# Kernel tuning notes

Hardware: AMD Instinct MI355X
Metric: run time of the kernel (lower is better)

Reference implementation:

```python
import jax, jax.numpy as jnp
import numpy as np
import math

H, N2, RANK, CH, LMAX = 256, 64, 1, 1, 2048
DT_MIN, DT_MAX = 1e-3, 1e-1


def setup_inputs() -> dict:
    key = jax.random.key(0)
    kP, kPi, kC, kCi, kdt = jax.random.split(key, 5)
    # DPLR 'lin' init: A = -1/2 - i*pi*n  (real_part=0.5, imag_part=pi*arange(N//2))
    A_real = 0.5 * jnp.ones((H, N2), jnp.float32)
    A_imag = math.pi * jnp.broadcast_to(jnp.arange(N2, dtype=jnp.float32), (H, N2))
    # B_init='constant': B = ones (complex)
    B_real = jnp.ones((H, N2), jnp.float32)
    B_imag = jnp.zeros((H, N2), jnp.float32)
    # P = randn complex (rank, H, N//2); torch complex randn has per-component std 1/sqrt(2)
    s = 1.0 / math.sqrt(2.0)
    P_real = s * jax.random.normal(kP, (RANK, H, N2), jnp.float32)
    P_imag = s * jax.random.normal(kPi, (RANK, H, N2), jnp.float32)
    # C (output projection) randn complex (channels, H, N//2)
    C_real = s * jax.random.normal(kC, (CH, H, N2), jnp.float32)
    C_imag = s * jax.random.normal(kCi, (CH, H, N2), jnp.float32)
    # dt log-uniform in [dt_min, dt_max]
    log_dt = math.log(DT_MIN) + jax.random.uniform(kdt, (H,), jnp.float32) * (
        math.log(DT_MAX) - math.log(DT_MIN))
    return {
        "A_real": A_real, "A_imag": A_imag,
        "B_real": B_real, "B_imag": B_imag,
        "P_real": P_real, "P_imag": P_imag,
        "C_real": C_real, "C_imag": C_imag,
        "log_dt": log_dt, "L": LMAX,
    }


def _krylov_doubling(dA, dB, L):
    """Matrix-power doubling scan (mirrors `power`): columns [dB, dA dB, ..., dA^{L-1} dB].

    dA: (H, N, N) complex, dB: (H, N) complex -> (H, N, L) complex.
    """
    x = dB[..., None]  # (H, N, 1)
    Ap = dA
    while x.shape[-1] < L:
        x = jnp.concatenate([x, Ap @ x], axis=-1)  # doubling step
        Ap = Ap @ Ap  # repeated squaring, as in power()
    return x[..., :L]


def reference(A_real, A_imag, B_real, B_imag, P_real, P_imag, C_real, C_imag, log_dt, L):
    # Build DPLR state matrix: A = diag(Lambda) - P P^*
    Lam = (-A_real - 1j * A_imag).astype(jnp.complex64)        # (H, N2)
    P = (P_real + 1j * P_imag).astype(jnp.complex64)           # (R, H, N2)
    B = (B_real + 1j * B_imag).astype(jnp.complex64)           # (H, N2)
    C = (C_real + 1j * C_imag).astype(jnp.complex64)           # (CH, H, N2)
    n2 = Lam.shape[-1]
    I = jnp.eye(n2, dtype=jnp.complex64)
    A_mat = Lam[:, :, None] * I - jnp.einsum('rhn,rhm->hnm', P, jnp.conj(P))  # (H,N2,N2)
    dt = jnp.exp(log_dt).astype(jnp.complex64)                 # (H,)
    # Bilinear (Tustin) discretization: dA = (I - dt/2 A)^{-1}(I + dt/2 A), dB = (I - dt/2 A)^{-1} dt B
    half = 0.5 * dt[:, None, None] * A_mat
    M_bwd = I - half
    dA = jnp.linalg.solve(M_bwd, I + half)                     # (H,N2,N2)
    dB = jnp.linalg.solve(M_bwd, (dt[:, None] * B)[..., None])[..., 0]  # (H,N2)
    # Kernel via power-doubling Krylov scan, then project: K[c,h,l] = 2 Re(C dA^l dB)
    x = _krylov_doubling(dA, dB, L)                            # (H,N2,L)
    K = 2.0 * jnp.real(jnp.einsum('chn,hnl->chl', C, x))       # (CH,H,L)
    return K
```

## Files before the change

kernel.cpp:

```cpp
#include <hip/hip_runtime.h>


#define LL 2048

struct C2 { float re, im; };

__device__ __forceinline__ C2 cmul(C2 a, C2 b){ return {a.re*b.re - a.im*b.im, a.re*b.im + a.im*b.re}; }
__device__ __forceinline__ C2 cadd(C2 a, C2 b){ return {a.re+b.re, a.im+b.im}; }
__device__ __forceinline__ C2 csub(C2 a, C2 b){ return {a.re-b.re, a.im-b.im}; }
__device__ __forceinline__ C2 cinv(C2 a){ float s=1.0f/(a.re*a.re+a.im*a.im); return {a.re*s, -a.im*s}; }
__device__ __forceinline__ C2 cscale(float s, C2 a){ return {s*a.re, s*a.im}; }
__device__ __forceinline__ C2 ld2(float2 v){ return {v.x, v.y}; }
__device__ __forceinline__ float2 st2(C2 v){ return make_float2(v.re, v.im); }

template<int CTRL>
__device__ __forceinline__ float dpp_add(float x){
  int t = __builtin_amdgcn_update_dpp(0, __float_as_int(x), CTRL, 0xF, 0xF, true);
  return x + __int_as_float(t);
}
__device__ __forceinline__ float wave_sum63(float x){
  x = dpp_add<0xB1>(x);
  x = dpp_add<0x4E>(x);
  x = dpp_add<0x124>(x);
  x = dpp_add<0x128>(x);
  x = dpp_add<0x142>(x);
  x = dpp_add<0x143>(x);
  return x;
}
__device__ __forceinline__ float bcast63(float x){
  return __int_as_float(__builtin_amdgcn_readlane(__float_as_int(x), 63));
}
__device__ __forceinline__ float rdlane(float v, int l){
  return __int_as_float(__builtin_amdgcn_readlane(__float_as_int(v), l));
}
__device__ __forceinline__ float shr1(float x){
  return __int_as_float(__builtin_amdgcn_update_dpp(0, __float_as_int(x), 0x138, 0xF, 0xF, true));
}
__device__ __forceinline__ float ins0(float v, float s, int lane){
  return (lane == 0) ? s : v;
}

__device__ __forceinline__ void tri_solve64(const C2 wl, C2 va, const int lane,
                                            float& so_re, float& so_im)
{
    C2 wsh = { shr1(wl.re), shr1(wl.im) };
    const float w0r = rdlane(wl.re, 0);
    const float w0i = rdlane(wl.im, 0);
    so_re = 0.0f; so_im = 0.0f;
    for (int j = 0; j < 64; j += 2) {
        const float s0r = rdlane(va.re, j);
        const float s0i = rdlane(va.im, j);
        const float v1r = rdlane(va.re, j + 1);
        const float v1i = rdlane(va.im, j + 1);
        const float s1r = v1r + (w0r*s0r - w0i*s0i);
        const float s1i = v1i + (w0r*s0i + w0i*s0r);
        if (lane == j)     { so_re = s0r; so_im = s0i; }
        if (lane == j + 1) { so_re = s1r; so_im = s1i; }
        const C2 wsh1 = { shr1(wsh.re), shr1(wsh.im) };
        va.re += wsh.re*s0r - wsh.im*s0i;
        va.im += wsh.re*s0i + wsh.im*s0r;
        va.re += wsh1.re*s1r - wsh1.im*s1i;
        va.im += wsh1.re*s1i + wsh1.im*s1r;
        wsh.re = shr1(wsh1.re);
        wsh.im = shr1(wsh1.im);
    }
}

__device__ __forceinline__ void tri_solve128(const C2 wlo, const C2 whi, const int lane,
                                             C2& tlo, C2& thi)
{
    C2 valo = wlo, vahi = whi;
    C2 wsl = { shr1(wlo.re), shr1(wlo.im) };
    C2 wsh;
    {
        const float br = rdlane(wlo.re, 63), bi = rdlane(wlo.im, 63);
        wsh.re = ins0(shr1(whi.re), br, lane);
        wsh.im = ins0(shr1(whi.im), bi, lane);
    }
    const float w0r = rdlane(wlo.re, 0);
    const float w0i = rdlane(wlo.im, 0);
    tlo = {0,0}; thi = {0,0};
    for (int j = 0; j < 64; j += 2) {
        const float s0r = rdlane(valo.re, j);
        const float s0i = rdlane(valo.im, j);
        const float v1r = rdlane(valo.re, j + 1);
        const float v1i = rdlane(valo.im, j + 1);
        const float s1r = v1r + (w0r*s0r - w0i*s0i);
        const float s1i = v1i + (w0r*s0i + w0i*s0r);
        if (lane == j)     { tlo.re = s0r; tlo.im = s0i; }
        if (lane == j + 1) { tlo.re = s1r; tlo.im = s1i; }
        const C2 wsl1 = { shr1(wsl.re), shr1(wsl.im) };
        C2 wsh1;
        {
            const float br = rdlane(wsl.re, 63), bi = rdlane(wsl.im, 63);
            wsh1.re = ins0(shr1(wsh.re), br, lane);
            wsh1.im = ins0(shr1(wsh.im), bi, lane);
        }
        valo.re += wsl.re*s0r - wsl.im*s0i + wsl1.re*s1r - wsl1.im*s1i;
        valo.im += wsl.re*s0i + wsl.im*s0r + wsl1.re*s1i + wsl1.im*s1r;
        vahi.re += wsh.re*s0r - wsh.im*s0i + wsh1.re*s1r - wsh1.im*s1i;
        vahi.im += wsh.re*s0i + wsh.im*s0r + wsh1.re*s1i + wsh1.im*s1r;
        wsl.re = shr1(wsl1.re); wsl.im = shr1(wsl1.im);
        {
            const float br = rdlane(wsl1.re, 63), bi = rdlane(wsl1.im, 63);
            wsh.re = ins0(shr1(wsh1.re), br, lane);
            wsh.im = ins0(shr1(wsh1.im), bi, lane);
        }
    }
    for (int j = 64; j < 128; j += 2) {
        const int jr = j - 64;
        const float s0r = rdlane(vahi.re, jr);
        const float s0i = rdlane(vahi.im, jr);
        const float v1r = rdlane(vahi.re, jr + 1);
        const float v1i = rdlane(vahi.im, jr + 1);
        const float s1r = v1r + (w0r*s0r - w0i*s0i);
        const float s1i = v1i + (w0r*s0i + w0i*s0r);
        if (lane == jr)     { thi.re = s0r; thi.im = s0i; }
        if (lane == jr + 1) { thi.re = s1r; thi.im = s1i; }
        const C2 wsh1 = { shr1(wsh.re), shr1(wsh.im) };
        vahi.re += wsh.re*s0r - wsh.im*s0i + wsh1.re*s1r - wsh1.im*s1i;
        vahi.im += wsh.re*s0i + wsh.im*s0r + wsh1.re*s1i + wsh1.im*s1r;
        wsh.re = shr1(wsh1.re);
        wsh.im = shr1(wsh1.im);
    }
}

__global__ __launch_bounds__(512)
__attribute__((amdgpu_waves_per_eu(2, 2)))
void ssm_dplr_kernel(
    const float* __restrict__ A_real, const float* __restrict__ A_imag,
    const float* __restrict__ B_real, const float* __restrict__ B_imag,
    const float* __restrict__ P_real, const float* __restrict__ P_imag,
    const float* __restrict__ C_real, const float* __restrict__ C_imag,
    const float* __restrict__ log_dt, float* __restrict__ out)
{
    const int h    = blockIdx.x;
    const int t    = threadIdx.x;
    const int lane = t & 63;
    const int wid  = t >> 6;

    extern __shared__ char sm[];
    float2* Abuf = (float2*)sm;
    float2* Cs   = (float2*)(sm + 32768);
    float2* tw   = Cs;
    float2* ta   = Cs + 512;
    float2* te   = Cs + 1024;
    float2* gA   = (float2*)(sm + 49152);
    float2* qA   = gA + 64;
    float2* g64A = gA + 128;
    float2* TgA  = gA + 192;
    float2* TpA  = gA + 256;
    float2* T1gA = gA + 320;
    float2* T1pA = gA + 384;
    char* ovl = sm + 52736;
    float2* rqA  = (float2*)ovl;
    float2* rxA  = rqA + 64;
    float2* reA  = rqA + 128;
    float2* wvA  = rqA + 192;
    float2* avA  = rqA + 256;
    float2* weA  = rqA + 320;
    float2* cbufAll = (float2*)ovl;
    float2* prtC    = (float2*)(sm + 56832);
    int*    cntA    = (int*)(sm + 65024);
    int*    cntB    = cntA + 32;

    const int idx = h * 64 + lane;
    const float dt = expf(log_dt[h]);
    const float c  = 0.5f * dt;

    const C2 lam = { -A_real[idx], -A_imag[idx] };
    const C2 p   = {  P_real[idx],  P_imag[idx] };
    const C2 Bv  = {  B_real[idx],  B_imag[idx] };
    const C2 Cv  = {  C_real[idx],  C_imag[idx] };
    const C2 pc  = { p.re, -p.im };

    const C2 d = cinv(C2{ 1.0f - c*lam.re, -c*lam.im });
    const C2 g = cmul(d, C2{ 1.0f + c*lam.re, c*lam.im });

    C2 sv = cscale(p.re*p.re + p.im*p.im, d);
    C2 uv = cmul(cmul(d, pc), Bv);
    sv.re = bcast63(wave_sum63(sv.re)); sv.im = bcast63(wave_sum63(sv.im));
    uv.re = bcast63(wave_sum63(uv.re)); uv.im = bcast63(wave_sum63(uv.im));

    const C2 beta  = cscale(c, cinv(C2{ 1.0f + c*sv.re, c*sv.im }));
    const C2 bs    = cmul(beta, sv);
    const C2 gamma = { -c*(1.0f - bs.re), c*bs.im };

    const C2 q  = cmul(d, p);
    const C2 r  = cmul(pc, csub(gamma, cmul(beta, g)));
    const C2 x0 = cscale(dt, csub(cmul(d, Bv), cmul(cmul(beta, uv), q)));

    const C2 g2  = cmul(g,  g);
    const C2 g4  = cmul(g2, g2);
    const C2 g8  = cmul(g4, g4);
    const C2 g16 = cmul(g8, g8);
    const C2 g32 = cmul(g16,g16);
    const C2 g64 = cmul(g32,g32);

    if (wid == 0) {
        const C2 rq = cmul(r, q);
        gA[lane]   = st2(g);
        qA[lane]   = st2(q);
        g64A[lane] = st2(g64);
        rqA[lane]  = st2(rq);
        rxA[lane]  = st2(cmul(r, x0));
        reA[lane]  = st2(cmul(rq, g64));
    }
    __syncthreads();

    {
        C2 cur = {1.0f, 0.0f};
        if (wid & 1) cur = g8;
        if (wid & 2) cur = cmul(cur, g16);
        if (wid & 4) cur = cmul(cur, g32);
        #pragma unroll
        for (int jj = 0; jj < 8; ++jj) {
            const int j = 8*wid + jj;
            Abuf[j*64 + ((lane + j) & 63)] = st2(cur);
            cur = cmul(cur, g);
        }
    }
    __syncthreads();

    {
        C2 accw = {0,0}, acca = {0,0}, acce = {0,0};
        #pragma unroll
        for (int kk = 0; kk < 8; ++kk) {
            const int n = 8*wid + kk;
            const C2 Gv = ld2(Abuf[lane*64 + ((n + lane) & 63)]);
            const C2 fq = ld2(rqA[n]);
            const C2 fx = ld2(rxA[n]);
            const C2 fe = ld2(reA[n]);
            accw = cadd(accw, cmul(Gv, fq));
            acca = cadd(acca, cmul(Gv, fx));
            acce = cadd(acce, cmul(Gv, fe));
        }
        tw[wid*64 + lane] = st2(accw);
        ta[wid*64 + lane] = st2(acca);
        te[wid*64 + lane] = st2(acce);
    }
    __syncthreads();
    if (t < 64) {
        C2 sw = {0,0}, sa = {0,0}, se = {0,0};
        #pragma unroll
        for (int w2 = 0; w2 < 8; ++w2) {
            sw = cadd(sw, ld2(tw[w2*64 + t]));
            sa = cadd(sa, ld2(ta[w2*64 + t]));
            se = cadd(se, ld2(te[w2*64 + t]));
        }
        wvA[t] = st2(sw);
        avA[t] = st2(sa);
        weA[t] = st2(se);
    }
    __syncthreads();

    const bool isB = (wid >= 4);
    const int  wg  = wid & 3;
    if (wid == 0) {
        C2 tlo, thi;
        tri_solve128(ld2(wvA[lane]), ld2(weA[lane]), lane, tlo, thi);
        C2 pp = { rdlane(tlo.re, 0),  rdlane(tlo.im, 0)  };
        C2 dd = {0,0};
        C2 qq = { rdlane(tlo.re, 63), rdlane(tlo.im, 63) };
        C2 qd = {0,0};
        for (int i = 1; i <= 63; ++i) {
            if (i <= 62) {
                const C2 ti = { rdlane(tlo.re, i), rdlane(tlo.im, i) };
                dd = cadd(cmul(dd, g), pp);
                pp = cadd(cmul(pp, g), ti);
            }
            const C2 tq = { rdlane(thi.re, i-1), rdlane(thi.im, i-1) };
            qd = cadd(cmul(qd, g), qq);
            qq = cadd(cmul(qq, g), tq);
        }
        const C2 T64v = cmul(g, pp);
        const C2 T64d = cadd(pp, cmul(g, dd));
        const C2 g63h  = cmul(g64, cinv(g));
        const C2 T128v = cadd(cmul(g64, T64v), cmul(g, qq));
        const C2 T128d = cadd(cadd(cscale(64.0f, cmul(g63h, T64v)), cmul(g64, T64d)),
                              cadd(qq, cmul(g, qd)));
        TgA[lane]  = st2(T64v);
        TpA[lane]  = st2(T64d);
        T1gA[lane] = st2(T128v);
        T1pA[lane] = st2(T128d);
    } else if (wid == 1) {
        float sg_re, sg_im;
        tri_solve64(ld2(wvA[lane]), ld2(avA[lane]), lane, sg_re, sg_im);
        C2 x = x0;
        for (int j = 0; j < 64; ++j) {
            Abuf[j*64 + ((lane + j) & 63)] = st2(x);
            const float sjr = rdlane(sg_re, j);
            const float sji = rdlane(sg_im, j);
            const float nr = g.re*x.re - g.im*x.im + sjr*q.re - sji*q.im;
            const float ni = g.re*x.im + g.im*x.re + sjr*q.im + sji*q.re;
            x.re = nr; x.im = ni;
        }
    }
    __syncthreads();

    C2 Mk[16];
    auto buildM = [&](bool p128){
        const C2 gt   = p128 ? cmul(g64, g64) : g64;
        const C2 Ttm  = p128 ? ld2(T1gA[lane]) : ld2(TgA[lane]);
        const C2 Tp   = p128 ? ld2(T1pA[lane]) : ld2(TpA[lane]);
        const C2 g63  = cmul(g64, cinv(g));
        const C2 gtm1 = p128 ? cmul(g64, g63) : g63;
        const C2 S    = cmul(r, cadd(cscale(p128 ? 128.0f : 64.0f, gtm1), Tp));
        const C2 diagv = cadd(gt, cmul(q, S));
        #pragma unroll
        for (int kk = 0; kk < 16; ++kk) {
            const int k = 16*wg + kk;
            const C2 qn   = ld2(qA[k]);
            const C2 g64n = ld2(g64A[k]);
            const C2 gtn  = p128 ? cmul(g64n, g64n) : g64n;
            const C2 Ttn  = p128 ? ld2(T1gA[k]) : ld2(TgA[k]);
            const C2 idm  = cinv(csub(ld2(gA[k]), g));
            const C2 num  = cmul(r, cadd(csub(gtn, gt), csub(Ttn, Ttm)));
            const C2 off  = cmul(cmul(qn, num), idm);
            const bool isd = (lane == k);
            Mk[kk].re = isd ? diagv.re : off.re;
            Mk[kk].im = isd ? diagv.im : off.im;
        }
    };
    if (!isB) buildM(true);
    else      buildM(false);
    if (wid == 0) Cs[lane] = st2(Cv);
    if (wid == 2) {
        if (lane < 32) cntA[lane] = 0;
        else           cntB[lane - 32] = 0;
    }
    __syncthreads();

    {
        float2* cb = cbufAll + wid*64;
        const float4* cb4 = (const float4*)cb;
        volatile int* vcnt = isB ? (volatile int*)cntB : (volatile int*)cntA;
        int* cnt = isB ? cntB : cntA;
        const int base = isB ? 4 : 0;
        cb[lane] = st2(Cv);

        const int s0 = isB ? 0 : 1;
        for (int s = s0; s <= 15; ++s) {
            const int buf = s & 1;
            float ar = 0.0f, ai = 0.0f;
            #pragma unroll
            for (int kp = 0; kp < 8; ++kp) {
                const float4 cc = cb4[8*wg + kp];
                ar += cc.x*Mk[2*kp].re   - cc.y*Mk[2*kp].im;
                ai += cc.x*Mk[2*kp].im   + cc.y*Mk[2*kp].re;
                ar += cc.z*Mk[2*kp+1].re - cc.w*Mk[2*kp+1].im;
                ai += cc.z*Mk[2*kp+1].im + cc.w*Mk[2*kp+1].re;
            }
            prtC[buf*512 + (base + wg)*64 + lane] = make_float2(ar, ai);
            __threadfence_block();
            if (lane == 0) atomicAdd(&cnt[s], 1);
            while (vcnt[s] < 4) { }
            __asm__ volatile("" ::: "memory");
            C2 nc = {0,0};
            #pragma unroll
            for (int w2 = 0; w2 < 4; ++w2) {
                const float2 pv = prtC[buf*512 + (base + w2)*64 + lane];
                nc.re += pv.x; nc.im += pv.y;
            }
            cb[lane] = st2(nc);
            if (!isB) {
                if (wid == 0) Cs[(2*s)*64 + lane] = st2(nc);
            } else {
                if (wid == 4) Cs[(2*s + 1)*64 + lane] = st2(nc);
                if (s == 0) buildM(true);
            }
        }
    }
    __syncthreads();

    {
        float accK[4] = {0.0f, 0.0f, 0.0f, 0.0f};
        #pragma unroll 8
        for (int n = 0; n < 64; ++n) {
            const float2 xv = Abuf[lane*64 + ((n + lane) & 63)];
            #pragma unroll
            for (int rr = 0; rr < 4; ++rr) {
                const float2 cv = Cs[(4*wid + rr)*64 + n];
                accK[rr] += cv.x*xv.x - cv.y*xv.y;
            }
        }
        float* outh = out + h * LL;
        #pragma unroll
        for (int rr = 0; rr < 4; ++rr) {
            outh[(4*wid + rr)*64 + lane] = 2.0f * accK[rr];
        }
    }
}

extern "C" void kernel_launch(void* const* d_in, const int* in_sizes, int n_in,
                              void* d_out, int out_size, void* d_ws, size_t ws_size,
                              hipStream_t stream) {
    const float* A_real = (const float*)d_in[0];
    const float* A_imag = (const float*)d_in[1];
    const float* B_real = (const float*)d_in[2];
    const float* B_imag = (const float*)d_in[3];
    const float* P_real = (const float*)d_in[4];
    const float* P_imag = (const float*)d_in[5];
    const float* C_real = (const float*)d_in[6];
    const float* C_imag = (const float*)d_in[7];
    const float* log_dt = (const float*)d_in[8];
    float* out = (float*)d_out;

    const size_t lds = 65280;
    ssm_dplr_kernel<<<256, 512, lds, stream>>>(
        A_real, A_imag, B_real, B_imag, P_real, P_imag,
        C_real, C_imag, log_dt, out);
}
```

Before: 106.1 us.

## Double block to 1024 threads and split C-recurrence across eight waves per chain

```diff
diff --git a/kernel.cpp b/kernel.cpp
--- a/kernel.cpp
+++ b/kernel.cpp
@@ -125,8 +125,8 @@
     }
 }
 
-__global__ __launch_bounds__(512)
-__attribute__((amdgpu_waves_per_eu(2, 2)))
+__global__ __launch_bounds__(1024)
+__attribute__((amdgpu_waves_per_eu(4, 4)))
 void ssm_dplr_kernel(
     const float* __restrict__ A_real, const float* __restrict__ A_imag,
     const float* __restrict__ B_real, const float* __restrict__ B_imag,
@@ -141,10 +141,13 @@
 
     extern __shared__ char sm[];
     float2* Abuf = (float2*)sm;
+    float2* cbufAll = (float2*)sm;
+    float2* prtC    = (float2*)(sm + 8192);
+    int*    cntA    = (int*)(sm + 24576);
+    int*    cntB    = cntA + 32;
     float2* Cs   = (float2*)(sm + 32768);
     float2* tw   = Cs;
-    float2* ta   = Cs + 512;
-    float2* te   = Cs + 1024;
+    float2* ta   = Cs + 1024;
     float2* gA   = (float2*)(sm + 49152);
     float2* qA   = gA + 64;
     float2* g64A = gA + 128;
@@ -152,17 +155,12 @@
     float2* TpA  = gA + 256;
     float2* T1gA = gA + 320;
     float2* T1pA = gA + 384;
-    char* ovl = sm + 52736;
-    float2* rqA  = (float2*)ovl;
+    float2* rqA  = (float2*)(sm + 52736);
     float2* rxA  = rqA + 64;
     float2* reA  = rqA + 128;
     float2* wvA  = rqA + 192;
     float2* avA  = rqA + 256;
     float2* weA  = rqA + 320;
-    float2* cbufAll = (float2*)ovl;
-    float2* prtC    = (float2*)(sm + 56832);
-    int*    cntA    = (int*)(sm + 65024);
-    int*    cntB    = cntA + 32;
 
     const int idx = h * 64 + lane;
     const float dt = expf(log_dt[h]);
@@ -210,12 +208,13 @@
 
     {
         C2 cur = {1.0f, 0.0f};
-        if (wid & 1) cur = g8;
-        if (wid & 2) cur = cmul(cur, g16);
-        if (wid & 4) cur = cmul(cur, g32);
-        #pragma unroll
-        for (int jj = 0; jj < 8; ++jj) {
-            const int j = 8*wid + jj;
+        if (wid & 1) cur = g4;
+        if (wid & 2) cur = cmul(cur, g8);
+        if (wid & 4) cur = cmul(cur, g16);
+        if (wid & 8) cur = cmul(cur, g32);
+        #pragma unroll
+        for (int jj = 0; jj < 4; ++jj) {
+            const int j = 4*wid + jj;
             Abuf[j*64 + ((lane + j) & 63)] = st2(cur);
             cur = cmul(cur, g);
         }
@@ -223,39 +222,62 @@
     __syncthreads();
 
     {
-        C2 accw = {0,0}, acca = {0,0}, acce = {0,0};
-        #pragma unroll
-        for (int kk = 0; kk < 8; ++kk) {
-            const int n = 8*wid + kk;
+        C2 accw = {0,0}, acca = {0,0};
+        #pragma unroll
+        for (int kk = 0; kk < 4; ++kk) {
+            const int n = 4*wid + kk;
             const C2 Gv = ld2(Abuf[lane*64 + ((n + lane) & 63)]);
             const C2 fq = ld2(rqA[n]);
             const C2 fx = ld2(rxA[n]);
-            const C2 fe = ld2(reA[n]);
             accw = cadd(accw, cmul(Gv, fq));
             acca = cadd(acca, cmul(Gv, fx));
-            acce = cadd(acce, cmul(Gv, fe));
         }
         tw[wid*64 + lane] = st2(accw);
         ta[wid*64 + lane] = st2(acca);
-        te[wid*64 + lane] = st2(acce);
     }
     __syncthreads();
     if (t < 64) {
-        C2 sw = {0,0}, sa = {0,0}, se = {0,0};
-        #pragma unroll
-        for (int w2 = 0; w2 < 8; ++w2) {
+        C2 sw = {0,0}, sa = {0,0};
+        #pragma unroll
+        for (int w2 = 0; w2 < 16; ++w2) {
             sw = cadd(sw, ld2(tw[w2*64 + t]));
             sa = cadd(sa, ld2(ta[w2*64 + t]));
-            se = cadd(se, ld2(te[w2*64 + t]));
         }
         wvA[t] = st2(sw);
         avA[t] = st2(sa);
+    }
+    __syncthreads();
+
+    {
+        C2 acce = {0,0};
+        #pragma unroll
+        for (int kk = 0; kk < 4; ++kk) {
+            const int n = 4*wid + kk;
+            const C2 Gv = ld2(Abuf[lane*64 + ((n + lane) & 63)]);
+            const C2 fe = ld2(reA[n]);
+            acce = cadd(acce, cmul(Gv, fe));
+        }
+        tw[wid*64 + lane] = st2(acce);
+    }
+    __syncthreads();
+    if (t < 64) {
+        C2 se = {0,0};
+        #pragma unroll
+        for (int w2 = 0; w2 < 16; ++w2) {
+            se = cadd(se, ld2(tw[w2*64 + t]));
+        }
         weA[t] = st2(se);
     }
     __syncthreads();
 
-    const bool isB = (wid >= 4);
-    const int  wg  = wid & 3;
+    const bool isB = (wid >= 8);
+    const int  dw  = wid & 7;
+    C2 idmk[8];
+    #pragma unroll
+    for (int kk = 0; kk < 8; ++kk) {
+        idmk[kk] = cinv(csub(ld2(gA[8*dw + kk]), g));
+    }
+    float sg_re = 0.0f, sg_im = 0.0f;
     if (wid == 0) {
         C2 tlo, thi;
         tri_solve128(ld2(wvA[lane]), ld2(weA[lane]), lane, tlo, thi);
@@ -284,8 +306,88 @@
         T1gA[lane] = st2(T128v);
         T1pA[lane] = st2(T128d);
     } else if (wid == 1) {
-        float sg_re, sg_im;
         tri_solve64(ld2(wvA[lane]), ld2(avA[lane]), lane, sg_re, sg_im);
+    } else if (wid == 2) {
+        if (lane < 32) cntA[lane] = 0;
+        else           cntB[lane - 32] = 0;
+    }
+    __syncthreads();
+
+    C2 Mk[8];
+    auto buildM = [&](bool p128){
+        const C2 gt   = p128 ? cmul(g64, g64) : g64;
+        const C2 Ttm  = p128 ? ld2(T1gA[lane]) : ld2(TgA[lane]);
+        const C2 Tp   = p128 ? ld2(T1pA[lane]) : ld2(TpA[lane]);
+        const C2 g63  = cmul(g64, cinv(g));
+        const C2 gtm1 = p128 ? cmul(g64, g63) : g63;
+        const C2 S    = cmul(r, cadd(cscale(p128 ? 128.0f : 64.0f, gtm1), Tp));
+        const C2 diagv = cadd(gt, cmul(q, S));
+        #pragma unroll
+        for (int kk = 0; kk < 8; ++kk) {
+            const int k = 8*dw + kk;
+            const C2 qn   = ld2(qA[k]);
+            const C2 g64n = ld2(g64A[k]);
+            const C2 gtn  = p128 ? cmul(g64n, g64n) : g64n;
+            const C2 Ttn  = p128 ? ld2(T1gA[k]) : ld2(TgA[k]);
+            const C2 num  = cmul(r, cadd(csub(gtn, gt), csub(Ttn, Ttm)));
+            const C2 off  = cmul(cmul(qn, num), idmk[kk]);
+            const bool isd = (lane == k);
+            Mk[kk].re = isd ? diagv.re : off.re;
+            Mk[kk].im = isd ? diagv.im : off.im;
+        }
+    };
+    if (!isB) buildM(true);
+    else      buildM(false);
+    if (wid == 0) Cs[lane] = st2(Cv);
+    __syncthreads();
+
+    {
+        float2* cb = cbufAll + wid*64;
+        const float4* cb4 = (const float4*)cb;
+        volatile int* vcnt = isB ? (volatile int*)cntB : (volatile int*)cntA;
+        int* cnt = isB ? cntB : cntA;
+        const int dbase = isB ? 8 : 0;
+        cb[lane] = st2(Cv);
+
+        const int s0 = isB ? 0 : 1;
+        for (int s = s0; s <= 15; ++s) {
+            const int buf = s & 1;
+            const float4 ya = cb4[4*dw + 0];
+            const float4 yb = cb4[4*dw + 1];
+            const float4 yc = cb4[4*dw + 2];
+            const float4 yd = cb4[4*dw + 3];
+            float ar = 0.0f, ai = 0.0f;
+            ar += ya.x*Mk[0].re - ya.y*Mk[0].im;  ai += ya.x*Mk[0].im + ya.y*Mk[0].re;
+            ar += ya.z*Mk[1].re - ya.w*Mk[1].im;  ai += ya.z*Mk[1].im + ya.w*Mk[1].re;
+            ar += yb.x*Mk[2].re - yb.y*Mk[2].im;  ai += yb.x*Mk[2].im + yb.y*Mk[2].re;
+            ar += yb.z*Mk[3].re - yb.w*Mk[3].im;  ai += yb.z*Mk[3].im + yb.w*Mk[3].re;
+            ar += yc.x*Mk[4].re - yc.y*Mk[4].im;  ai += yc.x*Mk[4].im + yc.y*Mk[4].re;
+            ar += yc.z*Mk[5].re - yc.w*Mk[5].im;  ai += yc.z*Mk[5].im + yc.w*Mk[5].re;
+            ar += yd.x*Mk[6].re - yd.y*Mk[6].im;  ai += yd.x*Mk[6].im + yd.y*Mk[6].re;
+            ar += yd.z*Mk[7].re - yd.w*Mk[7].im;  ai += yd.z*Mk[7].im + yd.w*Mk[7].re;
+            prtC[buf*1024 + (dbase + dw)*64 + lane] = make_float2(ar, ai);
+            __threadfence_block();
+            if (lane == 0) atomicAdd(&cnt[s], 1);
+            while (vcnt[s] < 8) { }
+            __asm__ volatile("" ::: "memory");
+            C2 nc = {0,0};
+            #pragma unroll
+            for (int w2 = 0; w2 < 8; ++w2) {
+                const float2 pv = prtC[buf*1024 + (dbase + w2)*64 + lane];
+                nc.re += pv.x; nc.im += pv.y;
+            }
+            cb[lane] = st2(nc);
+            if (!isB) {
+                if (wid == 0) Cs[(2*s)*64 + lane] = st2(nc);
+            } else {
+                if (wid == 8) Cs[(2*s + 1)*64 + lane] = st2(nc);
+                if (s == 0) buildM(true);
+            }
+        }
+    }
+    __syncthreads();
+
+    if (wid == 1) {
         C2 x = x0;
         for (int j = 0; j < 64; ++j) {
             Abuf[j*64 + ((lane + j) & 63)] = st2(x);
@@ -298,97 +400,20 @@
     }
     __syncthreads();
 
-    C2 Mk[16];
-    auto buildM = [&](bool p128){
-        const C2 gt   = p128 ? cmul(g64, g64) : g64;
-        const C2 Ttm  = p128 ? ld2(T1gA[lane]) : ld2(TgA[lane]);
-        const C2 Tp   = p128 ? ld2(T1pA[lane]) : ld2(TpA[lane]);
-        const C2 g63  = cmul(g64, cinv(g));
-        const C2 gtm1 = p128 ? cmul(g64, g63) : g63;
-        const C2 S    = cmul(r, cadd(cscale(p128 ? 128.0f : 64.0f, gtm1), Tp));
-        const C2 diagv = cadd(gt, cmul(q, S));
-        #pragma unroll
-        for (int kk = 0; kk < 16; ++kk) {
-            const int k = 16*wg + kk;
-            const C2 qn   = ld2(qA[k]);
-            const C2 g64n = ld2(g64A[k]);
-            const C2 gtn  = p128 ? cmul(g64n, g64n) : g64n;
-            const C2 Ttn  = p128 ? ld2(T1gA[k]) : ld2(TgA[k]);
-            const C2 idm  = cinv(csub(ld2(gA[k]), g));
-            const C2 num  = cmul(r, cadd(csub(gtn, gt), csub(Ttn, Ttm)));
-            const C2 off  = cmul(cmul(qn, num), idm);
-            const bool isd = (lane == k);
-            Mk[kk].re = isd ? diagv.re : off.re;
-            Mk[kk].im = isd ? diagv.im : off.im;
-        }
-    };
-    if (!isB) buildM(true);
-    else      buildM(false);
-    if (wid == 0) Cs[lane] = st2(Cv);
-    if (wid == 2) {
-        if (lane < 32) cntA[lane] = 0;
-        else           cntB[lane - 32] = 0;
-    }
-    __syncthreads();
-
-    {
-        float2* cb = cbufAll + wid*64;
-        const float4* cb4 = (const float4*)cb;
-        volatile int* vcnt = isB ? (volatile int*)cntB : (volatile int*)cntA;
-        int* cnt = isB ? cntB : cntA;
-        const int base = isB ? 4 : 0;
-        cb[lane] = st2(Cv);
-
-        const int s0 = isB ? 0 : 1;
-        for (int s = s0; s <= 15; ++s) {
-            const int buf = s & 1;
-            float ar = 0.0f, ai = 0.0f;
-            #pragma unroll
-            for (int kp = 0; kp < 8; ++kp) {
-                const float4 cc = cb4[8*wg + kp];
-                ar += cc.x*Mk[2*kp].re   - cc.y*Mk[2*kp].im;
-                ai += cc.x*Mk[2*kp].im   + cc.y*Mk[2*kp].re;
-                ar += cc.z*Mk[2*kp+1].re - cc.w*Mk[2*kp+1].im;
-                ai += cc.z*Mk[2*kp+1].im + cc.w*Mk[2*kp+1].re;
-            }
-            prtC[buf*512 + (base + wg)*64 + lane] = make_float2(ar, ai);
-            __threadfence_block();
-            if (lane == 0) atomicAdd(&cnt[s], 1);
-            while (vcnt[s] < 4) { }
-            __asm__ volatile("" ::: "memory");
-            C2 nc = {0,0};
-            #pragma unroll
-            for (int w2 = 0; w2 < 4; ++w2) {
-                const float2 pv = prtC[buf*512 + (base + w2)*64 + lane];
-                nc.re += pv.x; nc.im += pv.y;
-            }
-            cb[lane] = st2(nc);
-            if (!isB) {
-                if (wid == 0) Cs[(2*s)*64 + lane] = st2(nc);
-            } else {
-                if (wid == 4) Cs[(2*s + 1)*64 + lane] = st2(nc);
-                if (s == 0) buildM(true);
-            }
-        }
-    }
-    __syncthreads();
-
-    {
-        float accK[4] = {0.0f, 0.0f, 0.0f, 0.0f};
+    {
+        const int r0 = 2*wid, r1 = 2*wid + 1;
+        float a0 = 0.0f, a1 = 0.0f;
         #pragma unroll 8
         for (int n = 0; n < 64; ++n) {
             const float2 xv = Abuf[lane*64 + ((n + lane) & 63)];
-            #pragma unroll
-            for (int rr = 0; rr < 4; ++rr) {
-                const float2 cv = Cs[(4*wid + rr)*64 + n];
-                accK[rr] += cv.x*xv.x - cv.y*xv.y;
-            }
+            const float2 c0 = Cs[r0*64 + n];
+            const float2 c1 = Cs[r1*64 + n];
+            a0 += c0.x*xv.x - c0.y*xv.y;
+            a1 += c1.x*xv.x - c1.y*xv.y;
         }
         float* outh = out + h * LL;
-        #pragma unroll
-        for (int rr = 0; rr < 4; ++rr) {
-            outh[(4*wid + rr)*64 + lane] = 2.0f * accK[rr];
-        }
+        outh[r0*64 + lane] = 2.0f * a0;
+        outh[r1*64 + lane] = 2.0f * a1;
     }
 }
 
@@ -406,8 +431,8 @@
     const float* log_dt = (const float*)d_in[8];
     float* out = (float*)d_out;
 
-    const size_t lds = 65280;
-    ssm_dplr_kernel<<<256, 512, lds, stream>>>(
+    const size_t lds = 55808;
+    ssm_dplr_kernel<<<256, 1024, lds, stream>>>(
         A_real, A_imag, B_real, B_imag, P_real, P_imag,
         C_real, C_imag, log_dt, out);
 }
```

Result: no change. 107.3 us (+1.2%).
